# Optimization experiments

Hardware: AMD Instinct MI355X
Metric: run time of the kernel (lower is better)

The kernel has to match this reference:

```python
import jax, jax.numpy as jnp
import numpy as np

N_NEWS = 200000
N_COMPANIES = 10000
N_EDGES = 640000
HIDDEN = 256


def setup_inputs() -> dict:
    key = jax.random.key(0)
    ks = jax.random.split(key, 7)
    scale = 1.0 / np.sqrt(HIDDEN)  # keep tanh out of full saturation
    news_x = jax.random.normal(ks[0], (N_NEWS, HIDDEN), dtype=jnp.float32)
    company_x = jax.random.normal(ks[1], (N_COMPANIES, HIDDEN), dtype=jnp.float32)
    W_news = jax.random.normal(ks[2], (HIDDEN, HIDDEN), dtype=jnp.float32) * scale
    W_company = jax.random.normal(ks[3], (HIDDEN, HIDDEN), dtype=jnp.float32) * scale
    v = jax.random.normal(ks[4], (HIDDEN,), dtype=jnp.float32) * scale
    src = jax.random.randint(ks[5], (N_EDGES,), 0, N_NEWS, dtype=jnp.int64)
    dst = jax.random.randint(ks[6], (N_EDGES,), 0, N_COMPANIES, dtype=jnp.int64)
    return {
        "news_x": news_x,
        "company_x": company_x,
        "W_news": W_news,
        "W_company": W_company,
        "v": v,
        "src": src,
        "dst": dst,
        "num_companies": N_COMPANIES,
    }


def reference(news_x, company_x, W_news, W_company, v, src, dst, num_companies):
    # Gather per-edge endpoint features, project (nn.Linear applies x @ W.T).
    news_part = news_x[src] @ W_news.T          # [E, H]
    company_part = company_x[dst] @ W_company.T  # [E, H]
    scores = jnp.tanh(news_part + company_part) @ v  # [E]

    # Segment-wise (per-company) numerically stable softmax over incoming edges.
    smax = jax.ops.segment_max(scores, dst, num_segments=num_companies)  # [C]
    scores_exp = jnp.exp(scores - smax[dst])                             # [E]
    denom = jax.ops.segment_sum(scores_exp, dst, num_segments=num_companies)[dst]
    weights = scores_exp / jnp.clip(denom, 1e-9)                         # [E]

    # Weighted scatter-add of raw news features into company slots.
    out = jax.ops.segment_sum(news_x[src] * weights[:, None], dst,
                              num_segments=num_companies)               # [C, H]
    return out
```

## Files before the change

### kernel.cpp

```cpp
#include <hip/hip_runtime.h>
#include <hip/hip_bf16.h>
#include <cmath>
#include <cstdint>


#define H 256

typedef __attribute__((ext_vector_type(8))) short bfrag;
typedef __attribute__((ext_vector_type(4))) float ffrag;

__device__ __forceinline__ ushort f2bf(float f) {
  uint u = __float_as_uint(f);
  uint r = u + 0x7FFFu + ((u >> 16) & 1u);
  return (ushort)(r >> 16);
}
__device__ __forceinline__ float bf2f(ushort h) {
  return __uint_as_float((uint)h << 16);
}

__global__ void prep_kernel(const float* __restrict__ Wn, const float* __restrict__ Wc,
                            ushort* __restrict__ WnHi, ushort* __restrict__ WnLo,
                            ushort* __restrict__ WcHi, ushort* __restrict__ WcLo,
                            const int* __restrict__ dst, int* __restrict__ counts, int E) {
  const int b = blockIdx.x, tid = threadIdx.x;
  if (b < 256) {
    int i = b * 256 + tid;
    float w = Wn[i];
    ushort h = f2bf(w);
    WnHi[i] = h;
    WnLo[i] = f2bf(w - bf2f(h));
  } else if (b < 512) {
    int i = (b - 256) * 256 + tid;
    float w = Wc[i];
    ushort h = f2bf(w);
    WcHi[i] = h;
    WcLo[i] = f2bf(w - bf2f(h));
  } else {
    int e = (b - 512) * 256 + tid;
    if (e < E) atomicAdd(&counts[dst[e]], 1);
  }
}

__global__ void scan_kernel(const int* __restrict__ counts, int* __restrict__ offsets,
                            int* __restrict__ cursor, int C) {
  __shared__ int wsum[4];
  int tid = threadIdx.x;
  int lane = tid & 63, wid = tid >> 6;
  int base = 0;
  for (int start = 0; start < C; start += 256) {
    int idx = start + tid;
    int val = (idx < C) ? counts[idx] : 0;
    int x = val;
#pragma unroll
    for (int off = 1; off < 64; off <<= 1) {
      int y = __shfl_up(x, off);
      if (lane >= off) x += y;
    }
    if (lane == 63) wsum[wid] = x;
    __syncthreads();
    int add = base;
    for (int w = 0; w < wid; ++w) add += wsum[w];
    if (idx < C) {
      int excl = add + x - val;
      offsets[idx] = excl;
      cursor[idx]  = excl;
    }
    int tot = wsum[0] + wsum[1] + wsum[2] + wsum[3];
    __syncthreads();
    base += tot;
  }
  if (tid == 0) offsets[C] = base;
}

__global__ void fill_kernel(const int* __restrict__ src, const int* __restrict__ dst,
                            int* __restrict__ cursor, int* __restrict__ srcs_sorted, int E) {
  int e = blockIdx.x * blockDim.x + threadIdx.x;
  if (e < E) {
    int d = dst[e];
    int pos = atomicAdd(&cursor[d], 1);
    srcs_sorted[pos] = src[e];
  }
}

__global__ __launch_bounds__(256, 2) void gemm_mfma2(
    const float* __restrict__ X, const ushort* __restrict__ Whi,
    const ushort* __restrict__ Wlo, ushort* __restrict__ projbf,
    ushort* __restrict__ xbf, int M) {
  constexpr int PITCH = 264;
  __shared__ ushort Xs[64 * PITCH];
  const int tid = threadIdx.x;
  const int wave = tid >> 6, lane = tid & 63;
  const int q = lane >> 4, nidx = lane & 15;
  const int row0 = blockIdx.x * 64;

#pragma unroll
  for (int it = 0; it < 8; ++it) {
    const int flat = it * 2048 + tid * 8;
    const int r = flat >> 8, k = flat & 255;
    int gr = row0 + r;
    if (gr >= M) gr = M - 1;
    const float4 x0 = *(const float4*)(X + (size_t)gr * H + k);
    const float4 x1 = *(const float4*)(X + (size_t)gr * H + k + 4);
    bfrag xb;
    xb[0] = (short)f2bf(x0.x); xb[1] = (short)f2bf(x0.y);
    xb[2] = (short)f2bf(x0.z); xb[3] = (short)f2bf(x0.w);
    xb[4] = (short)f2bf(x1.x); xb[5] = (short)f2bf(x1.y);
    xb[6] = (short)f2bf(x1.z); xb[7] = (short)f2bf(x1.w);
    *(bfrag*)&Xs[r * PITCH + k] = xb;
    if (xbf) *(bfrag*)(xbf + (size_t)gr * H + k) = xb;
  }
  __syncthreads();

  ffrag acc[4][4];
#pragma unroll
  for (int i = 0; i < 4; ++i)
#pragma unroll
    for (int t = 0; t < 4; ++t) acc[i][t] = (ffrag)(0.f);

#pragma unroll
  for (int ks = 0; ks < 8; ++ks) {
    const int k0 = ks * 32;
    bfrag a[4];
#pragma unroll
    for (int i = 0; i < 4; ++i)
      a[i] = *(const bfrag*)&Xs[(16 * i + nidx) * PITCH + k0 + q * 8];
    bfrag bhi[4], blo[4];
#pragma unroll
    for (int t = 0; t < 4; ++t) {
      const size_t off = (size_t)(wave * 64 + t * 16 + nidx) * H + k0 + q * 8;
      bhi[t] = *(const bfrag*)(Whi + off);
      blo[t] = *(const bfrag*)(Wlo + off);
    }
#pragma unroll
    for (int i = 0; i < 4; ++i)
#pragma unroll
      for (int t = 0; t < 4; ++t) {
        acc[i][t] = __builtin_amdgcn_mfma_f32_16x16x32_bf16(a[i], bhi[t], acc[i][t], 0, 0, 0);
        acc[i][t] = __builtin_amdgcn_mfma_f32_16x16x32_bf16(a[i], blo[t], acc[i][t], 0, 0, 0);
      }
  }

#pragma unroll
  for (int i = 0; i < 4; ++i)
#pragma unroll
    for (int r = 0; r < 4; ++r) {
      const int grow = row0 + 16 * i + q * 4 + r;
      if (grow < M) {
#pragma unroll
        for (int t = 0; t < 4; ++t)
          projbf[(size_t)grow * H + wave * 64 + t * 16 + nidx] = f2bf(acc[i][t][r]);
      }
    }
}

__device__ __forceinline__ float fast_tanh(float x) {
  float e = __expf(2.f * x);
  return 1.f - 2.f / (e + 1.f);
}

__device__ __forceinline__ float score_dot(ushort4 p, float4 cq, float4 vv) {
  float r = fast_tanh(bf2f(p.x) + cq.x) * vv.x + fast_tanh(bf2f(p.y) + cq.y) * vv.y +
            fast_tanh(bf2f(p.z) + cq.z) * vv.z + fast_tanh(bf2f(p.w) + cq.w) * vv.w;
#pragma unroll
  for (int off = 32; off > 0; off >>= 1) r += __shfl_xor(r, off);
  return r;
}

__global__ __launch_bounds__(256) void edge_flash_kernel(
    const ushort* __restrict__ news_projbf, const ushort* __restrict__ company_projbf,
    const float* __restrict__ v, const int* __restrict__ offsets,
    const int* __restrict__ srcs, const ushort* __restrict__ news_xbf,
    float* __restrict__ out) {
  const int c = blockIdx.x;
  const int tid = threadIdx.x, lane = tid & 63, wid = tid >> 6;
  __shared__ float cp[H];
  __shared__ float mW[4], lW[4];
  __shared__ float OW[4][H];
  cp[tid] = bf2f(company_projbf[(size_t)c * H + tid]);
  __syncthreads();
  const float4 vv = *(const float4*)(v + lane * 4);
  const float4 cq = *(const float4*)&cp[lane * 4];
  const int beg = offsets[c], end = offsets[c + 1];

  float m = -INFINITY, l = 0.f;
  float4 O = make_float4(0.f, 0.f, 0.f, 0.f);

  int i = beg + wid * 2;
  if (i + 1 < end) {
    int s0 = srcs[i], s1 = srcs[i + 1];
    ushort4 p0 = *(const ushort4*)(news_projbf + (size_t)s0 * H + lane * 4);
    ushort4 p1 = *(const ushort4*)(news_projbf + (size_t)s1 * H + lane * 4);
    ushort4 x0 = *(const ushort4*)(news_xbf + (size_t)s0 * H + lane * 4);
    ushort4 x1 = *(const ushort4*)(news_xbf + (size_t)s1 * H + lane * 4);
    for (;;) {
      const int inext = i + 8;
      const bool more = (inext + 1 < end);
      ushort4 np0, np1, nx0, nx1;
      if (more) {
        int t0 = srcs[inext], t1 = srcs[inext + 1];
        np0 = *(const ushort4*)(news_projbf + (size_t)t0 * H + lane * 4);
        np1 = *(const ushort4*)(news_projbf + (size_t)t1 * H + lane * 4);
        nx0 = *(const ushort4*)(news_xbf + (size_t)t0 * H + lane * 4);
        nx1 = *(const ushort4*)(news_xbf + (size_t)t1 * H + lane * 4);
      }
      const float sa = score_dot(p0, cq, vv);
      const float sb = score_dot(p1, cq, vv);
      const float mnew = fmaxf(m, fmaxf(sa, sb));
      const float alpha = __expf(m - mnew);
      const float pa = __expf(sa - mnew);
      const float pb = __expf(sb - mnew);
      l = l * alpha + pa + pb;
      O.x = O.x * alpha + pa * bf2f(x0.x) + pb * bf2f(x1.x);
      O.y = O.y * alpha + pa * bf2f(x0.y) + pb * bf2f(x1.y);
      O.z = O.z * alpha + pa * bf2f(x0.z) + pb * bf2f(x1.z);
      O.w = O.w * alpha + pa * bf2f(x0.w) + pb * bf2f(x1.w);
      m = mnew;
      i = inext;
      if (!more) break;
      p0 = np0; p1 = np1; x0 = nx0; x1 = nx1;
    }
  }
  if (i < end) {
    const int s0 = srcs[i];
    const ushort4 p0 = *(const ushort4*)(news_projbf + (size_t)s0 * H + lane * 4);
    const ushort4 x0 = *(const ushort4*)(news_xbf + (size_t)s0 * H + lane * 4);
    const float sa = score_dot(p0, cq, vv);
    const float mnew = fmaxf(m, sa);
    const float alpha = __expf(m - mnew);
    const float pa = __expf(sa - mnew);
    l = l * alpha + pa;
    O.x = O.x * alpha + pa * bf2f(x0.x);
    O.y = O.y * alpha + pa * bf2f(x0.y);
    O.z = O.z * alpha + pa * bf2f(x0.z);
    O.w = O.w * alpha + pa * bf2f(x0.w);
    m = mnew;
  }

  if (lane == 0) { mW[wid] = m; lW[wid] = l; }
  *(float4*)&OW[wid][lane * 4] = O;
  __syncthreads();
  const float mstar = fmaxf(fmaxf(mW[0], mW[1]), fmaxf(mW[2], mW[3]));
  float denom = 0.f, val = 0.f;
#pragma unroll
  for (int w = 0; w < 4; ++w) {
    const float sc = (lW[w] > 0.f) ? __expf(mW[w] - mstar) : 0.f;
    denom += lW[w] * sc;
    val += OW[w][tid] * sc;
  }
  out[(size_t)c * H + tid] = val / fmaxf(denom, 1e-9f);
}

extern "C" void kernel_launch(void* const* d_in, const int* in_sizes, int n_in,
                              void* d_out, int out_size, void* d_ws, size_t ws_size,
                              hipStream_t stream) {
  const float* news_x    = (const float*)d_in[0];
  const float* company_x = (const float*)d_in[1];
  const float* W_news    = (const float*)d_in[2];
  const float* W_company = (const float*)d_in[3];
  const float* v         = (const float*)d_in[4];
  const int*   src       = (const int*)d_in[5];
  const int*   dst       = (const int*)d_in[6];
  const int N = in_sizes[0] / H;
  const int C = in_sizes[1] / H;
  const int E = in_sizes[5];
  float* out = (float*)d_out;

  char* p = (char*)d_ws;
  ushort* news_projbf    = (ushort*)p; p += (size_t)N * H * sizeof(ushort);
  ushort* news_xbf       = (ushort*)p; p += (size_t)N * H * sizeof(ushort);
  ushort* company_projbf = (ushort*)p; p += (size_t)C * H * sizeof(ushort);
  int*    srcs_sorted    = (int*)p;    p += (size_t)E * sizeof(int);
  ushort* Wn_hi          = (ushort*)p; p += (size_t)H * H * sizeof(ushort);
  ushort* Wn_lo          = (ushort*)p; p += (size_t)H * H * sizeof(ushort);
  ushort* Wc_hi          = (ushort*)p; p += (size_t)H * H * sizeof(ushort);
  ushort* Wc_lo          = (ushort*)p; p += (size_t)H * H * sizeof(ushort);
  int*    counts         = (int*)p;    p += (size_t)C * sizeof(int);
  int*    offsets        = (int*)p;    p += (size_t)(C + 1) * sizeof(int);
  int*    cursor         = (int*)p;    p += (size_t)C * sizeof(int);

  hipMemsetAsync(counts, 0, (size_t)C * sizeof(int), stream);
  prep_kernel<<<512 + (E + 255) / 256, 256, 0, stream>>>(
      W_news, W_company, Wn_hi, Wn_lo, Wc_hi, Wc_lo, dst, counts, E);
  scan_kernel<<<1, 256, 0, stream>>>(counts, offsets, cursor, C);
  fill_kernel<<<(E + 255) / 256, 256, 0, stream>>>(src, dst, cursor, srcs_sorted, E);

  gemm_mfma2<<<(C + 63) / 64, 256, 0, stream>>>(company_x, Wc_hi, Wc_lo,
                                                company_projbf, (ushort*)nullptr, C);
  gemm_mfma2<<<(N + 63) / 64, 256, 0, stream>>>(news_x, Wn_hi, Wn_lo,
                                                news_projbf, news_xbf, N);

  edge_flash_kernel<<<C, 256, 0, stream>>>(news_projbf, company_projbf, v, offsets,
                                           srcs_sorted, news_xbf, out);
}
```

Measured before the change: 659.1 us.

## Convert inputs to bf16 in prep kernel and feed GEMM directly from global

The fp32-to-bf16 conversion of news_x and company_x moves out of the GEMM into the prep kernel. A new GEMM kernel reads bf16 A fragments straight from global memory instead of staging them through LDS, with no shared memory and launch bounds raised to 4 blocks per CU. This removes the LDS staging and barrier and is meant to raise occupancy. In exchange, news_x gets an extra bf16 round trip through global memory (the GEMM previously wrote xbf as a side effect, now it re-reads it), and each wave reloads A fragments from global/L2 with no LDS reuse.

```diff
diff --git a/kernel.cpp b/kernel.cpp
--- a/kernel.cpp
+++ b/kernel.cpp
@@ -21,7 +21,11 @@
 __global__ void prep_kernel(const float* __restrict__ Wn, const float* __restrict__ Wc,
                             ushort* __restrict__ WnHi, ushort* __restrict__ WnLo,
                             ushort* __restrict__ WcHi, ushort* __restrict__ WcLo,
-                            const int* __restrict__ dst, int* __restrict__ counts, int E) {
+                            const int* __restrict__ dst, int* __restrict__ counts, int E,
+                            const float* __restrict__ news_x, ushort* __restrict__ news_xbf,
+                            long nNewsElems,
+                            const float* __restrict__ company_x, ushort* __restrict__ company_xbf,
+                            long nCompElems, int nbE, int nbN) {
   const int b = blockIdx.x, tid = threadIdx.x;
   if (b < 256) {
     int i = b * 256 + tid;
@@ -35,9 +39,26 @@
     ushort h = f2bf(w);
     WcHi[i] = h;
     WcLo[i] = f2bf(w - bf2f(h));
-  } else {
+  } else if (b < 512 + nbE) {
     int e = (b - 512) * 256 + tid;
     if (e < E) atomicAdd(&counts[dst[e]], 1);
+  } else {
+    const bool news = (b < 512 + nbE + nbN);
+    const long base = news ? ((long)(b - 512 - nbE) * 2048 + (long)tid * 8)
+                           : ((long)(b - 512 - nbE - nbN) * 2048 + (long)tid * 8);
+    const float* srcp = news ? news_x : company_x;
+    ushort* dstp = news ? news_xbf : company_xbf;
+    const long total = news ? nNewsElems : nCompElems;
+    if (base + 8 <= total) {
+      const float4 x0 = *(const float4*)(srcp + base);
+      const float4 x1 = *(const float4*)(srcp + base + 4);
+      bfrag xb;
+      xb[0] = (short)f2bf(x0.x); xb[1] = (short)f2bf(x0.y);
+      xb[2] = (short)f2bf(x0.z); xb[3] = (short)f2bf(x0.w);
+      xb[4] = (short)f2bf(x1.x); xb[5] = (short)f2bf(x1.y);
+      xb[6] = (short)f2bf(x1.z); xb[7] = (short)f2bf(x1.w);
+      *(bfrag*)(dstp + base) = xb;
+    }
   }
 }
 
@@ -82,61 +103,53 @@
   }
 }
 
-__global__ __launch_bounds__(256, 2) void gemm_mfma2(
-    const float* __restrict__ X, const ushort* __restrict__ Whi,
-    const ushort* __restrict__ Wlo, ushort* __restrict__ projbf,
-    ushort* __restrict__ xbf, int M) {
-  constexpr int PITCH = 264;
-  __shared__ ushort Xs[64 * PITCH];
+__global__ __launch_bounds__(256, 4) void gemm_direct(
+    const ushort* __restrict__ Xbf, const ushort* __restrict__ Whi,
+    const ushort* __restrict__ Wlo, ushort* __restrict__ projbf, int M) {
   const int tid = threadIdx.x;
   const int wave = tid >> 6, lane = tid & 63;
   const int q = lane >> 4, nidx = lane & 15;
   const int row0 = blockIdx.x * 64;
 
-#pragma unroll
-  for (int it = 0; it < 8; ++it) {
-    const int flat = it * 2048 + tid * 8;
-    const int r = flat >> 8, k = flat & 255;
-    int gr = row0 + r;
-    if (gr >= M) gr = M - 1;
-    const float4 x0 = *(const float4*)(X + (size_t)gr * H + k);
-    const float4 x1 = *(const float4*)(X + (size_t)gr * H + k + 4);
-    bfrag xb;
-    xb[0] = (short)f2bf(x0.x); xb[1] = (short)f2bf(x0.y);
-    xb[2] = (short)f2bf(x0.z); xb[3] = (short)f2bf(x0.w);
-    xb[4] = (short)f2bf(x1.x); xb[5] = (short)f2bf(x1.y);
-    xb[6] = (short)f2bf(x1.z); xb[7] = (short)f2bf(x1.w);
-    *(bfrag*)&Xs[r * PITCH + k] = xb;
-    if (xbf) *(bfrag*)(xbf + (size_t)gr * H + k) = xb;
-  }
-  __syncthreads();
-
   ffrag acc[4][4];
 #pragma unroll
   for (int i = 0; i < 4; ++i)
 #pragma unroll
     for (int t = 0; t < 4; ++t) acc[i][t] = (ffrag)(0.f);
 
-#pragma unroll
+  const ushort* arow[4];
+#pragma unroll
+  for (int i = 0; i < 4; ++i) {
+    int r = row0 + 16 * i + nidx;
+    if (r >= M) r = M - 1;
+    arow[i] = Xbf + (size_t)r * H + q * 8;
+  }
+  const ushort* bhirow[4];
+  const ushort* blorow[4];
+#pragma unroll
+  for (int t = 0; t < 4; ++t) {
+    const size_t off = (size_t)(wave * 64 + t * 16 + nidx) * H + q * 8;
+    bhirow[t] = Whi + off;
+    blorow[t] = Wlo + off;
+  }
+
+#pragma unroll 2
   for (int ks = 0; ks < 8; ++ks) {
     const int k0 = ks * 32;
-    bfrag a[4];
+    bfrag a[4], bh[4], bl[4];
+#pragma unroll
+    for (int i = 0; i < 4; ++i) a[i] = *(const bfrag*)(arow[i] + k0);
+#pragma unroll
+    for (int t = 0; t < 4; ++t) {
+      bh[t] = *(const bfrag*)(bhirow[t] + k0);
+      bl[t] = *(const bfrag*)(blorow[t] + k0);
+    }
 #pragma unroll
     for (int i = 0; i < 4; ++i)
-      a[i] = *(const bfrag*)&Xs[(16 * i + nidx) * PITCH + k0 + q * 8];
-    bfrag bhi[4], blo[4];
-#pragma unroll
-    for (int t = 0; t < 4; ++t) {
-      const size_t off = (size_t)(wave * 64 + t * 16 + nidx) * H + k0 + q * 8;
-      bhi[t] = *(const bfrag*)(Whi + off);
-      blo[t] = *(const bfrag*)(Wlo + off);
-    }
-#pragma unroll
-    for (int i = 0; i < 4; ++i)
 #pragma unroll
       for (int t = 0; t < 4; ++t) {
-        acc[i][t] = __builtin_amdgcn_mfma_f32_16x16x32_bf16(a[i], bhi[t], acc[i][t], 0, 0, 0);
-        acc[i][t] = __builtin_amdgcn_mfma_f32_16x16x32_bf16(a[i], blo[t], acc[i][t], 0, 0, 0);
+        acc[i][t] = __builtin_amdgcn_mfma_f32_16x16x32_bf16(a[i], bh[t], acc[i][t], 0, 0, 0);
+        acc[i][t] = __builtin_amdgcn_mfma_f32_16x16x32_bf16(a[i], bl[t], acc[i][t], 0, 0, 0);
       }
   }
 
@@ -269,6 +282,7 @@
   ushort* news_projbf    = (ushort*)p; p += (size_t)N * H * sizeof(ushort);
   ushort* news_xbf       = (ushort*)p; p += (size_t)N * H * sizeof(ushort);
   ushort* company_projbf = (ushort*)p; p += (size_t)C * H * sizeof(ushort);
+  ushort* company_xbf    = (ushort*)p; p += (size_t)C * H * sizeof(ushort);
   int*    srcs_sorted    = (int*)p;    p += (size_t)E * sizeof(int);
   ushort* Wn_hi          = (ushort*)p; p += (size_t)H * H * sizeof(ushort);
   ushort* Wn_lo          = (ushort*)p; p += (size_t)H * H * sizeof(ushort);
@@ -278,16 +292,23 @@
   int*    offsets        = (int*)p;    p += (size_t)(C + 1) * sizeof(int);
   int*    cursor         = (int*)p;    p += (size_t)C * sizeof(int);
 
+  const long nNewsElems = (long)N * H;
+  const long nCompElems = (long)C * H;
+  const int nbE = (E + 255) / 256;
+  const int nbN = (int)((nNewsElems + 2047) / 2048);
+  const int nbC = (int)((nCompElems + 2047) / 2048);
+
   hipMemsetAsync(counts, 0, (size_t)C * sizeof(int), stream);
-  prep_kernel<<<512 + (E + 255) / 256, 256, 0, stream>>>(
-      W_news, W_company, Wn_hi, Wn_lo, Wc_hi, Wc_lo, dst, counts, E);
+  prep_kernel<<<512 + nbE + nbN + nbC, 256, 0, stream>>>(
+      W_news, W_company, Wn_hi, Wn_lo, Wc_hi, Wc_lo, dst, counts, E,
+      news_x, news_xbf, nNewsElems, company_x, company_xbf, nCompElems, nbE, nbN);
   scan_kernel<<<1, 256, 0, stream>>>(counts, offsets, cursor, C);
   fill_kernel<<<(E + 255) / 256, 256, 0, stream>>>(src, dst, cursor, srcs_sorted, E);
 
-  gemm_mfma2<<<(C + 63) / 64, 256, 0, stream>>>(company_x, Wc_hi, Wc_lo,
-                                                company_projbf, (ushort*)nullptr, C);
-  gemm_mfma2<<<(N + 63) / 64, 256, 0, stream>>>(news_x, Wn_hi, Wn_lo,
-                                                news_projbf, news_xbf, N);
+  gemm_direct<<<(C + 63) / 64, 256, 0, stream>>>(company_xbf, Wc_hi, Wc_lo,
+                                                 company_projbf, C);
+  gemm_direct<<<(N + 63) / 64, 256, 0, stream>>>(news_xbf, Wn_hi, Wn_lo,
+                                                 news_projbf, N);
 
   edge_flash_kernel<<<C, 256, 0, stream>>>(news_projbf, company_projbf, v, offsets,
                                            srcs_sorted, news_xbf, out);
```

Measured after the change: 815.6 us. 23.7% more time.
